# Performance work log

Hardware: AMD Instinct MI355X
Metric: run time of the kernel (lower is better)

Reference implementation:

```python
import jax, jax.numpy as jnp
import numpy as np

N, T, D, C = 32, 512, 1024, 120
EPS = 1e-12
SCALE = 2.0 * (D ** 0.5)


def setup_inputs() -> dict:
    key = jax.random.key(0)
    ks = jax.random.split(key, 16)
    inp = {
        'anc_perm_input': jax.random.normal(ks[0], (N, T, D), dtype=jnp.float32),
        'pos_perm_input': jax.random.normal(ks[1], (N, T, D), dtype=jnp.float32),
        'neg_perm_input': jax.random.normal(ks[2], (N, T, D), dtype=jnp.float32),
        'anc_src_key_padding_mask': jax.random.randint(ks[3], (N, T), 0, 2) == 1,
        'pos_src_key_padding_mask': jax.random.randint(ks[4], (N, T), 0, 2) == 1,
        'neg_src_key_padding_mask': jax.random.randint(ks[5], (N, T), 0, 2) == 1,
        # learned parameters (stored as (in, out); math-equivalent to torch x @ W.T)
        'W_attn': jax.random.normal(ks[6], (D, D), dtype=jnp.float32) * 0.02,
        'b_attn': jnp.zeros((D,), dtype=jnp.float32),
        'W1': jax.random.normal(ks[7], (D, D), dtype=jnp.float32) * 0.02,
        'b1': jnp.zeros((D,), dtype=jnp.float32),
        'W2': jax.random.normal(ks[8], (D, D), dtype=jnp.float32) * 0.02,
        'b2': jnp.zeros((D,), dtype=jnp.float32),
        'ln_g': jnp.ones((D,), dtype=jnp.float32),
        'ln_b': jnp.zeros((D,), dtype=jnp.float32),
        'W_last': jax.random.normal(ks[9], (D, C), dtype=jnp.float32) * 0.02,
        'b_last': jnp.zeros((C,), dtype=jnp.float32),
    }
    return inp


def _ntd_nd(x, mask, W_attn, b_attn, W1, b1, W2, b2, ln_g, ln_b, W_last, b_last):
    # x: (N,T,D); mask: (N,T) bool, True = padding
    w = x @ W_attn + b_attn                                   # (N,T,D)
    valid = ~mask                                             # (N,T)
    scores = jnp.einsum('btd,bsd->bts', w, w)                 # (N,T,T)
    scores = jnp.where(valid[:, :, None] & valid[:, None, :], scores, 0.0)
    s = jnp.sum(scores, axis=1) / SCALE                       # (N,T)
    s = jnp.where(mask, -jnp.inf, s)
    attn = jax.nn.softmax(s, axis=1)                          # (N,T)
    # proj_head: duplicate OrderedDict key => linear1 -> relu -> linear2 (no final act)
    proj = jax.nn.relu(x @ W1 + b1) @ W2 + b2                 # (N,T,D)
    pooled = jnp.einsum('bt,btd->bd', attn, proj)             # (N,D)
    mu = jnp.mean(pooled, axis=-1, keepdims=True)
    var = jnp.var(pooled, axis=-1, keepdims=True)
    normed = (pooled - mu) / jnp.sqrt(var + EPS) * ln_g + ln_b
    return jax.nn.relu(normed) @ W_last + b_last              # (N,C)


def reference(anc_perm_input, pos_perm_input, neg_perm_input,
              anc_src_key_padding_mask, pos_src_key_padding_mask, neg_src_key_padding_mask,
              W_attn, b_attn, W1, b1, W2, b2, ln_g, ln_b, W_last, b_last):
    params = (W_attn, b_attn, W1, b1, W2, b2, ln_g, ln_b, W_last, b_last)
    anc = _ntd_nd(anc_perm_input, anc_src_key_padding_mask, *params)
    pos = _ntd_nd(pos_perm_input, pos_src_key_padding_mask, *params)
    neg = _ntd_nd(neg_perm_input, neg_src_key_padding_mask, *params)
    return (anc, pos, neg)
```

## Files before the change

kernel.cpp:

```cpp
#include <hip/hip_runtime.h>
#include <hip/hip_bf16.h>
#include <math.h>

#define N_B 32
#define T_S 512
#define D_D 1024
#define C_C 120
#define ZB 96
#define SCALE 64.0f

typedef unsigned short u16;
typedef __attribute__((ext_vector_type(8))) short short8;
typedef __attribute__((ext_vector_type(8))) unsigned short ushort8;
typedef __attribute__((ext_vector_type(4))) float floatx4;

__device__ inline u16 f2bf(float f) {
    union { __hip_bfloat16 h; u16 u; } c; c.h = __float2bfloat16(f); return c.u;
}
__device__ inline float bf2f(u16 u) {
    union { unsigned i; float f; } c; c.i = ((unsigned)u) << 16; return c.f;
}

__device__ inline void gll16(const void* g, void* l) {
    __builtin_amdgcn_global_load_lds((const __attribute__((address_space(1))) void*)g,
                                     (__attribute__((address_space(3))) void*)l,
                                     16, 0, 0);
}

__device__ inline bool mask_is_i8(const int* mk) {
    bool i8 = false;
#pragma unroll
    for (int i = 0; i < 16; i++) {
        unsigned v = ((const unsigned*)mk)[i];
        if (v > 1u) i8 = true;
    }
    return i8;
}
__device__ inline int mask_val(const int* mk, int idx, bool i8) {
    return i8 ? (int)((const signed char*)mk)[idx] : mk[idx];
}

__global__ __launch_bounds__(512)
void k_scan(const int* m0, const int* m1, const int* m2,
            const float* __restrict__ W_attn, const float* __restrict__ W1,
            int* __restrict__ slotbase, int* __restrict__ cnts,
            int* __restrict__ gb, int* __restrict__ zblk,
            int* __restrict__ mtot, u16* __restrict__ xp,
            float* __restrict__ WT, u16* __restrict__ W1T,
            float4* __restrict__ zreg) {
    int zb = blockIdx.x;
    int tid = threadIdx.x;
    if (zb >= ZB) {
        int bx = zb - ZB;
        int tbx = bx & 31, tby = bx >> 5;
        __shared__ float tile[32][33];
        int tx = tid & 31, ty = tid >> 5;
#pragma unroll
        for (int j = 0; j < 32; j += 16)
            tile[ty + j][tx] = W_attn[(size_t)(tby*32 + ty + j)*D_D + tbx*32 + tx];
        __syncthreads();
#pragma unroll
        for (int j = 0; j < 32; j += 16)
            WT[(size_t)(tbx*32 + ty + j)*D_D + tby*32 + tx] = tile[tx][ty + j];
        __syncthreads();
#pragma unroll
        for (int j = 0; j < 32; j += 16)
            tile[ty + j][tx] = W1[(size_t)(tby*32 + ty + j)*D_D + tbx*32 + tx];
        __syncthreads();
#pragma unroll
        for (int j = 0; j < 32; j += 16)
            W1T[(size_t)(tbx*32 + ty + j)*D_D + tby*32 + tx] = f2bf(tile[tx][ty + j]);
        return;
    }
    {
        float4 zz4 = {0.f, 0.f, 0.f, 0.f};
        for (int i = zb * 512 + tid; i < (2 * 1024 * 1024 / 16); i += ZB * 512)
            zreg[i] = zz4;
    }
    bool i8_0 = mask_is_i8(m0), i8_1 = mask_is_i8(m1), i8_2 = mask_is_i8(m2);
    __shared__ unsigned short wc[ZB][8];
    __shared__ int scnt[ZB], sgb[ZB], stot;
    int wave = tid >> 6, lane = tid & 63;
#pragma unroll
    for (int it = 0; it < 12; it++) {
        int zb2 = wave * 12 + it;
        int z2 = zb2 >> 5, b2 = zb2 & 31;
        const int* mk = z2 == 0 ? m0 : (z2 == 1 ? m1 : m2);
        bool i8 = z2 == 0 ? i8_0 : (z2 == 1 ? i8_1 : i8_2);
        int c = 0;
        if (i8) {
            const signed char* p = (const signed char*)mk + b2 * T_S + lane * 8;
#pragma unroll
            for (int e = 0; e < 8; e++) c += (p[e] == 0);
        } else {
            const int* p = mk + b2 * T_S + lane * 8;
#pragma unroll
            for (int e = 0; e < 8; e++) c += (p[e] == 0);
        }
        c += __shfl_xor(c, 1, 64);
        c += __shfl_xor(c, 2, 64);
        c += __shfl_xor(c, 4, 64);
        if ((lane & 7) == 0) wc[zb2][lane >> 3] = (unsigned short)c;
    }
    __syncthreads();
    if (tid < ZB) {
        int s = 0;
#pragma unroll
        for (int c = 0; c < 8; c++) s += wc[tid][c];
        scnt[tid] = s;
    }
    __syncthreads();
    if (tid == 0) {
        int run = 0;
        for (int i = 0; i < ZB; i++) { sgb[i] = run; run += (scnt[i] + 63) & ~63; }
        stot = run;
    }
    __syncthreads();
    int cnt = scnt[zb], base = sgb[zb];
    if (tid == 0) {
        cnts[zb] = cnt; gb[zb] = base;
        int run = base;
#pragma unroll
        for (int c = 0; c < 8; c++) { slotbase[zb * 8 + c] = run; run += wc[zb][c]; }
        if (zb == ZB - 1) mtot[0] = stot;
    }
    int nb = (cnt + 63) >> 6;
    if (tid < nb) zblk[(base >> 6) + tid] = zb;
    int cend = (cnt + 63) & ~63;
    {
        u16* bp = xp + (size_t)(base + cnt) * D_D;
        int n8 = (cend - cnt) * (D_D / 8);
        ushort8 zz = {0,0,0,0,0,0,0,0};
        for (int i = tid; i < n8; i += 512)
            *(ushort8*)(bp + (size_t)i * 8) = zz;
    }
    if (zb == ZB - 1) {
        int tot = stot, tend = (tot + 255) & ~255;
        u16* bp = xp + (size_t)tot * D_D;
        int n8 = (tend - tot) * (D_D / 8);
        ushort8 zz = {0,0,0,0,0,0,0,0};
        for (int i = tid; i < n8; i += 512)
            *(ushort8*)(bp + (size_t)i * 8) = zz;
        if (tid < ((tend - tot) >> 6)) zblk[(tot >> 6) + tid] = 0;
    }
}

__global__ void k_prep(const float* x0, const float* x1, const float* x2,
                       const int* m0, const int* m1, const int* m2,
                       const int* __restrict__ slotbase,
                       float* __restrict__ xsum, u16* __restrict__ xp) {
    int idx = blockIdx.x;
    int tid = threadIdx.x;
    int chunk = idx & 7, zb = idx >> 3;
    int z = zb >> 5, b = zb & 31;
    const float* x = z == 0 ? x0 : (z == 1 ? x1 : x2);
    const int* mk = z == 0 ? m0 : (z == 1 ? m1 : m2);
    bool i8 = mask_is_i8(mk);
    int t0 = chunk * 64;
    __shared__ unsigned char s_list[64];
    __shared__ int s_cc;
    if (tid < 64) {
        bool v = (mask_val(mk, b * T_S + t0 + tid, i8) == 0);
        unsigned long long bal = __ballot(v);
        int pos = (int)__popcll(bal & ((1ull << tid) - 1ull));
        if (v) s_list[pos] = (unsigned char)tid;
        if (tid == 0) s_cc = (int)__popcll(bal);
    }
    __syncthreads();
    int cc = s_cc;
    int slot0 = slotbase[zb * 8 + chunk];
    const float4* xr = (const float4*)(x + (size_t)(b * T_S) * D_D);
    float4 acc = {0.f, 0.f, 0.f, 0.f};
#pragma unroll 4
    for (int j = 0; j < cc; j++) {
        int t = t0 + (int)s_list[j];
        float4 v = xr[(size_t)t * 256 + tid];
        union { __hip_bfloat162 h; ushort2 u; } c0, c1;
        c0.h = __float22bfloat162_rn({v.x, v.y});
        c1.h = __float22bfloat162_rn({v.z, v.w});
        ushort4 uu = {c0.u.x, c0.u.y, c1.u.x, c1.u.y};
        *(ushort4*)(xp + (size_t)(slot0 + j) * D_D + tid * 4) = uu;
        acc.x += v.x; acc.y += v.y; acc.z += v.z; acc.w += v.w;
    }
    float* xs = xsum + (size_t)zb * D_D + tid * 4;
    atomicAdd(xs + 0, acc.x); atomicAdd(xs + 1, acc.y);
    atomicAdd(xs + 2, acc.z); atomicAdd(xs + 3, acc.w);
}

__global__ void k_matvec(const float* __restrict__ W, const float* __restrict__ vin,
                         const float* __restrict__ bias, const int* __restrict__ bmul,
                         float scale, float* __restrict__ vout) {
    int z = blockIdx.z, bg = blockIdx.y;
    int och = blockIdx.x >> 3, kc = blockIdx.x & 7;
    int o = och * 256 + threadIdx.x;
    int brow = z * N_B + bg * 8;
    float acc[8] = {0.f, 0.f, 0.f, 0.f, 0.f, 0.f, 0.f, 0.f};
    if (kc == 0 && bias) {
        float bv = bias[o];
#pragma unroll
        for (int bb = 0; bb < 8; bb++)
            acc[bb] = bmul ? bv * (float)bmul[brow + bb] : bv;
    }
    const float* vi = vin + (size_t)brow * D_D + kc * 128;
    const float* Wp = W + (size_t)(kc * 128) * D_D + o;
#pragma unroll 4
    for (int i = 0; i < 128; i++) {
        float wv = Wp[(size_t)i * D_D];
#pragma unroll
        for (int bb = 0; bb < 8; bb++)
            acc[bb] += vi[(size_t)bb * D_D + i] * wv;
    }
#pragma unroll
    for (int bb = 0; bb < 8; bb++)
        atomicAdd(&vout[(size_t)(brow + bb) * D_D + o], acc[bb] * scale);
}

__global__ void k_dots(const u16* __restrict__ xp, const float* __restrict__ vs,
                       const int* __restrict__ zblk, const int* __restrict__ mtot,
                       float* __restrict__ sdot) {
    int t0 = blockIdx.x * 4;
    if (t0 >= mtot[0]) return;
    int t = t0 + (threadIdx.x >> 6);
    int lane = threadIdx.x & 63;
    int zb = zblk[t0 >> 6];
    const u16* xr = xp + (size_t)t * D_D;
    const float* vr = vs + (size_t)zb * D_D;
    float acc = 0.f;
#pragma unroll
    for (int i = 0; i < 2; i++) {
        short8 v = *(const short8*)(xr + i * 512 + lane * 8);
        const float* vp = vr + i * 512 + lane * 8;
        float4 a0 = *(const float4*)(vp);
        float4 a1 = *(const float4*)(vp + 4);
        acc += bf2f((u16)v[0]) * a0.x + bf2f((u16)v[1]) * a0.y
             + bf2f((u16)v[2]) * a0.z + bf2f((u16)v[3]) * a0.w
             + bf2f((u16)v[4]) * a1.x + bf2f((u16)v[5]) * a1.y
             + bf2f((u16)v[6]) * a1.z + bf2f((u16)v[7]) * a1.w;
    }
#pragma unroll
    for (int off = 32; off; off >>= 1) acc += __shfl_xor(acc, off, 64);
    if (lane == 0) sdot[t] = acc;
}

#define STAGE_TILE(buf, k0)                                                   \
    {                                                                         \
        _Pragma("unroll")                                                     \
        for (int i_ = 0; i_ < 4; i_++) {                                      \
            int r0_ = i_ * 64 + wave * 8;                                     \
            int rr_ = r0_ + srow;                                             \
            int gc_ = cp ^ srow;            \
            gll16(abase + (size_t)rr_ * D_D + (k0) + gc_ * 8,                 \
                  &As[buf][r0_ * 64]);                                        \
            gll16(bbase + (size_t)rr_ * D_D + (k0) + gc_ * 8,                 \
                  &Bs[buf][r0_ * 64]);                                        \
        }                                                                     \
    }

__global__ __launch_bounds__(512, 1)
void k_gemm_bf16(const u16* __restrict__ xp, const u16* __restrict__ W1T,
                 const float* __restrict__ b1, const float* __restrict__ sdot,
                 const int* __restrict__ cnts, const int* __restrict__ gb,
                 const int* __restrict__ zblk, const int* __restrict__ mtot,
                 float* __restrict__ rbuf) {
    int bid = blockIdx.x;
    int sub = bid & 31;
    int Mt = (bid >> 5) * 8 + (sub & 7);
    int Nt = sub >> 3;
    int row0 = Mt * 256, N0 = Nt * 256;
    if (row0 >= mtot[0]) return;

    __shared__ __align__(16) u16 As[2][256 * 64];
    __shared__ __align__(16) u16 Bs[2][256 * 64];
    __shared__ float sAttn[256];
    __shared__ float redm[8], reds[8];
    int tid = threadIdx.x;
    int wave = tid >> 6, lane = tid & 63;

    {
        int g0 = row0 >> 6;
        int prevzb = -1, czb_cnt = 0, czb_base = 0;
        float mx = 0.f, tot = 1.f;
#pragma unroll
        for (int g = 0; g < 4; g++) {
            int zbg = zblk[g0 + g];
            if (zbg != prevzb) {
                czb_cnt = cnts[zbg]; czb_base = gb[zbg];
                float v = (tid < czb_cnt) ? sdot[czb_base + tid] : -INFINITY;
                float m = v;
#pragma unroll
                for (int off = 32; off; off >>= 1) m = fmaxf(m, __shfl_xor(m, off, 64));
                if (lane == 0) redm[wave] = m;
                __syncthreads();
                m = redm[0];
#pragma unroll
                for (int k = 1; k < 8; k++) m = fmaxf(m, redm[k]);
                float e = __expf(v - m);
#pragma unroll
                for (int off = 32; off; off >>= 1) e += __shfl_xor(e, off, 64);
                if (lane == 0) reds[wave] = e;
                __syncthreads();
                float t_ = 0.f;
#pragma unroll
                for (int k = 0; k < 8; k++) t_ += reds[k];
                mx = m; tot = t_; prevzb = zbg;
            }
            if (tid < 64) {
                int row = row0 + g * 64 + tid;
                int tl = row - czb_base;
                float w = 0.f;
                if (tl < czb_cnt) w = __expf(sdot[row] - mx) / tot;
                sAttn[g * 64 + tid] = w;
            }
            __syncthreads();
        }
    }

    int wy = wave >> 2, wx = wave & 3;
    int q = lane >> 4, cidx = lane & 15;
    int srow = lane >> 3;
    int cp = lane & 7;

    floatx4 acc[8][4];
#pragma unroll
    for (int mi = 0; mi < 8; mi++)
#pragma unroll
        for (int ni = 0; ni < 4; ni++)
            acc[mi][ni] = (floatx4){0.f, 0.f, 0.f, 0.f};

    const u16* abase = xp + (size_t)row0 * D_D;
    const u16* bbase = W1T + (size_t)N0 * D_D;

    STAGE_TILE(0, 0)
    __syncthreads();
    int cur = 0;
#pragma unroll 2
    for (int kt = 0; kt < 16; kt++) {
        if (kt < 15) { STAGE_TILE(cur ^ 1, (kt + 1) << 6) }
        __builtin_amdgcn_sched_barrier(0);
#pragma unroll
        for (int ks = 0; ks < 2; ks++) {
            short8 a[8], bfr[4];
#pragma unroll
            for (int mi = 0; mi < 8; mi++) {
                int m = wy * 128 + mi * 16 + cidx;
                a[mi] = *(const short8*)&As[cur][m * 64 + ((((ks << 2) | q) ^ (m & 7)) << 3)];
            }
#pragma unroll
            for (int ni = 0; ni < 4; ni++) {
                int n = wx * 64 + ni * 16 + cidx;
                bfr[ni] = *(const short8*)&Bs[cur][n * 64 + ((((ks << 2) | q) ^ (n & 7)) << 3)];
            }
#pragma unroll
            for (int mi = 0; mi < 8; mi++)
#pragma unroll
                for (int ni = 0; ni < 4; ni++)
                    acc[mi][ni] = __builtin_amdgcn_mfma_f32_16x16x32_bf16(
                        a[mi], bfr[ni], acc[mi][ni], 0, 0, 0);
        }
        __syncthreads();
        cur ^= 1;
    }

    int zb0 = zblk[(row0 >> 6) + wy * 2];
    int zb1 = zblk[(row0 >> 6) + wy * 2 + 1];
#pragma unroll
    for (int ni = 0; ni < 4; ni++) {
        int ng = N0 + wx * 64 + ni * 16 + cidx;
        float b1v = b1[ng];
        float s0 = 0.f, s1 = 0.f;
#pragma unroll
        for (int mi = 0; mi < 8; mi++) {
            float part = 0.f;
#pragma unroll
            for (int rg = 0; rg < 4; rg++) {
                int ml = wy * 128 + mi * 16 + q * 4 + rg;
                float hv = fmaxf(acc[mi][ni][rg] + b1v, 0.f);
                part += hv * sAttn[ml];
            }
            if (mi < 4) s0 += part; else s1 += part;
        }
        s0 += __shfl_xor(s0, 16, 64); s0 += __shfl_xor(s0, 32, 64);
        s1 += __shfl_xor(s1, 16, 64); s1 += __shfl_xor(s1, 32, 64);
        if (lane < 16) {
            atomicAdd(&rbuf[(size_t)zb0 * D_D + ng], s0);
            atomicAdd(&rbuf[(size_t)zb1 * D_D + ng], s1);
        }
    }
}

__global__ void k_fin(const float* __restrict__ pooled, const float* __restrict__ ln_g,
                      const float* __restrict__ ln_b, const float* __restrict__ Wl,
                      const float* __restrict__ bl, float* __restrict__ out) {
    int zb = blockIdx.x;
    int tid = threadIdx.x;
    __shared__ float nr[D_D];
    __shared__ float redA[8], redB[8];
    __shared__ float ps[4][C_C];
    const float* p = pooled + (size_t)zb * D_D;
    int o0 = tid, o1 = tid + 512;
    float a0 = p[o0], a1 = p[o1];
    float s1 = a0 + a1, s2 = a0 * a0 + a1 * a1;
#pragma unroll
    for (int off = 32; off; off >>= 1) {
        s1 += __shfl_xor(s1, off, 64);
        s2 += __shfl_xor(s2, off, 64);
    }
    int w = tid >> 6;
    if ((tid & 63) == 0) { redA[w] = s1; redB[w] = s2; }
    __syncthreads();
    float t1 = 0.f, t2 = 0.f;
#pragma unroll
    for (int k = 0; k < 8; k++) { t1 += redA[k]; t2 += redB[k]; }
    float mu = t1 * (1.0f / D_D);
    float var = t2 * (1.0f / D_D) - mu * mu;
    float rstd = 1.0f / sqrtf(var + 1e-12f);
    nr[o0] = fmaxf((a0 - mu) * rstd * ln_g[o0] + ln_b[o0], 0.f);
    nr[o1] = fmaxf((a1 - mu) * rstd * ln_g[o1] + ln_b[o1], 0.f);
    __syncthreads();
    if (tid < 4 * C_C) {
        int seg = tid / C_C, c = tid - seg * C_C;
        const float* wp = Wl + (size_t)(seg * 256) * C_C + c;
        const float* np = nr + seg * 256;
        float acc = 0.f;
#pragma unroll 8
        for (int d = 0; d < 256; d++)
            acc += np[d] * wp[(size_t)d * C_C];
        ps[seg][c] = acc;
    }
    __syncthreads();
    if (tid < C_C)
        out[(size_t)zb * C_C + tid] =
            bl[tid] + ps[0][tid] + ps[1][tid] + ps[2][tid] + ps[3][tid];
}

extern "C" void kernel_launch(void* const* d_in, const int* in_sizes, int n_in,
                              void* d_out, int out_size, void* d_ws, size_t ws_size,
                              hipStream_t stream) {
    const float* x0 = (const float*)d_in[0];
    const float* x1 = (const float*)d_in[1];
    const float* x2 = (const float*)d_in[2];
    const int* m0 = (const int*)d_in[3];
    const int* m1 = (const int*)d_in[4];
    const int* m2 = (const int*)d_in[5];
    const float* W_attn = (const float*)d_in[6];
    const float* b_attn = (const float*)d_in[7];
    const float* W1 = (const float*)d_in[8];
    const float* b1 = (const float*)d_in[9];
    const float* W2 = (const float*)d_in[10];
    const float* b2 = (const float*)d_in[11];
    const float* ln_g = (const float*)d_in[12];
    const float* ln_b = (const float*)d_in[13];
    const float* W_last = (const float*)d_in[14];
    const float* b_last = (const float*)d_in[15];
    float* out = (float*)d_out;

    char* wsb = (char*)d_ws;
    const size_t MB = 1 << 20;
    float* WT     = (float*)(wsb);
    u16*   W1T    = (u16*)  (wsb + 4 * MB);
    float* xsum   = (float*)(wsb + 6 * MB);
    float* rbuf   = (float*)(wsb + 6 * MB + 393216);
    float* wsum   = (float*)(wsb + 6 * MB + 786432);
    float* vs     = (float*)(wsb + 6 * MB + 1179648);
    float* pooled = (float*)(wsb + 6 * MB + 1572864);
    float* sdot   = (float*)(wsb + 8 * MB);
    int*   slotb  = (int*)  (wsb + 8 * MB + 524288);
    int*   cnts   = (int*)  (wsb + 8 * MB + 528384);
    int*   gb     = (int*)  (wsb + 8 * MB + 532480);
    int*   mtot   = (int*)  (wsb + 8 * MB + 536576);
    int*   zblk   = (int*)  (wsb + 8 * MB + 540672);
    u16*   xp     = (u16*)  (wsb + 9 * MB);

    k_scan  <<<ZB + 1024, 512, 0, stream>>>(m0, m1, m2, W_attn, W1,
                                            slotb, cnts, gb, zblk, mtot,
                                            xp, WT, W1T, (float4*)(wsb + 6 * MB));
    k_prep  <<<768, 256, 0, stream>>>(x0, x1, x2, m0, m1, m2, slotb, xsum, xp);
    k_matvec<<<dim3(32, 4, 3), 256, 0, stream>>>(W_attn, xsum, b_attn, cnts, 1.0f, wsum);
    k_matvec<<<dim3(32, 4, 3), 256, 0, stream>>>(WT, wsum, nullptr, nullptr, 1.0f / SCALE, vs);
    k_dots  <<<12288, 256, 0, stream>>>(xp, vs, zblk, mtot, sdot);
    k_gemm_bf16<<<768, 512, 0, stream>>>(xp, W1T, b1, sdot, cnts, gb, zblk, mtot, rbuf);
    k_matvec<<<dim3(32, 4, 3), 256, 0, stream>>>(W2, rbuf, b2, nullptr, 1.0f, pooled);
    k_fin   <<<ZB, 512, 0, stream>>>(pooled, ln_g, ln_b, W_last, b_last, out);
}
```

Measured before the change: 375.6 us.

## Merge matvec/dots and W2/LN-final stages into cooperative kernels with grid sync

Replaces the two attention matvec launches and the dots launch with one cooperative kernel that separates the stages with grid.sync. Likewise, the W2 matvec and the LayerNorm/final linear are merged into a second cooperative kernel, where the matvec now uses 512-thread blocks. The goal is to remove kernel launch gaps and the tail effects of small grids. In exchange it pays for grid-wide barriers, and the dots stage runs on a fixed 768-block persistent loop instead of 12288 blocks.

```diff
diff --git a/kernel.cpp b/kernel.cpp
--- a/kernel.cpp
+++ b/kernel.cpp
@@ -1,6 +1,9 @@
 #include <hip/hip_runtime.h>
 #include <hip/hip_bf16.h>
+#include <hip/hip_cooperative_groups.h>
 #include <math.h>
+
+namespace cg = cooperative_groups;
 
 #define N_B 32
 #define T_S 512
@@ -187,59 +190,85 @@
     atomicAdd(xs + 2, acc.z); atomicAdd(xs + 3, acc.w);
 }
 
-__global__ void k_matvec(const float* __restrict__ W, const float* __restrict__ vin,
-                         const float* __restrict__ bias, const int* __restrict__ bmul,
-                         float scale, float* __restrict__ vout) {
-    int z = blockIdx.z, bg = blockIdx.y;
-    int och = blockIdx.x >> 3, kc = blockIdx.x & 7;
-    int o = och * 256 + threadIdx.x;
-    int brow = z * N_B + bg * 8;
-    float acc[8] = {0.f, 0.f, 0.f, 0.f, 0.f, 0.f, 0.f, 0.f};
-    if (kc == 0 && bias) {
-        float bv = bias[o];
+__global__ __launch_bounds__(256)
+void k_mid(const float* __restrict__ W, const float* __restrict__ WT,
+           const float* __restrict__ b_attn, const int* __restrict__ cnts,
+           const float* __restrict__ xsum, float* __restrict__ wsum,
+           float* __restrict__ vs, const u16* __restrict__ xp,
+           const int* __restrict__ zblk, const int* __restrict__ mtot,
+           float* __restrict__ sdot) {
+    cg::grid_group grid = cg::this_grid();
+    int bid = blockIdx.x, tid = threadIdx.x;
+    if (bid < 384) {
+        int x = bid & 31, bg = (bid >> 5) & 3, z = bid >> 7;
+        int och = x >> 3, kc = x & 7;
+        int o = och * 256 + tid;
+        int brow = z * N_B + bg * 8;
+        float acc[8] = {0.f, 0.f, 0.f, 0.f, 0.f, 0.f, 0.f, 0.f};
+        if (kc == 0) {
+            float bv = b_attn[o];
+#pragma unroll
+            for (int bb = 0; bb < 8; bb++)
+                acc[bb] = bv * (float)cnts[brow + bb];
+        }
+        const float* vi = xsum + (size_t)brow * D_D + kc * 128;
+        const float* Wp = W + (size_t)(kc * 128) * D_D + o;
+#pragma unroll 4
+        for (int i = 0; i < 128; i++) {
+            float wv = Wp[(size_t)i * D_D];
+#pragma unroll
+            for (int bb = 0; bb < 8; bb++)
+                acc[bb] += vi[(size_t)bb * D_D + i] * wv;
+        }
 #pragma unroll
         for (int bb = 0; bb < 8; bb++)
-            acc[bb] = bmul ? bv * (float)bmul[brow + bb] : bv;
-    }
-    const float* vi = vin + (size_t)brow * D_D + kc * 128;
-    const float* Wp = W + (size_t)(kc * 128) * D_D + o;
+            atomicAdd(&wsum[(size_t)(brow + bb) * D_D + o], acc[bb]);
+    }
+    grid.sync();
+    if (bid < 384) {
+        int x = bid & 31, bg = (bid >> 5) & 3, z = bid >> 7;
+        int och = x >> 3, kc = x & 7;
+        int o = och * 256 + tid;
+        int brow = z * N_B + bg * 8;
+        float acc[8] = {0.f, 0.f, 0.f, 0.f, 0.f, 0.f, 0.f, 0.f};
+        const float* vi = wsum + (size_t)brow * D_D + kc * 128;
+        const float* Wp = WT + (size_t)(kc * 128) * D_D + o;
 #pragma unroll 4
-    for (int i = 0; i < 128; i++) {
-        float wv = Wp[(size_t)i * D_D];
+        for (int i = 0; i < 128; i++) {
+            float wv = Wp[(size_t)i * D_D];
+#pragma unroll
+            for (int bb = 0; bb < 8; bb++)
+                acc[bb] += vi[(size_t)bb * D_D + i] * wv;
+        }
 #pragma unroll
         for (int bb = 0; bb < 8; bb++)
-            acc[bb] += vi[(size_t)bb * D_D + i] * wv;
-    }
-#pragma unroll
-    for (int bb = 0; bb < 8; bb++)
-        atomicAdd(&vout[(size_t)(brow + bb) * D_D + o], acc[bb] * scale);
-}
-
-__global__ void k_dots(const u16* __restrict__ xp, const float* __restrict__ vs,
-                       const int* __restrict__ zblk, const int* __restrict__ mtot,
-                       float* __restrict__ sdot) {
-    int t0 = blockIdx.x * 4;
-    if (t0 >= mtot[0]) return;
-    int t = t0 + (threadIdx.x >> 6);
-    int lane = threadIdx.x & 63;
-    int zb = zblk[t0 >> 6];
-    const u16* xr = xp + (size_t)t * D_D;
-    const float* vr = vs + (size_t)zb * D_D;
-    float acc = 0.f;
-#pragma unroll
-    for (int i = 0; i < 2; i++) {
-        short8 v = *(const short8*)(xr + i * 512 + lane * 8);
-        const float* vp = vr + i * 512 + lane * 8;
-        float4 a0 = *(const float4*)(vp);
-        float4 a1 = *(const float4*)(vp + 4);
-        acc += bf2f((u16)v[0]) * a0.x + bf2f((u16)v[1]) * a0.y
-             + bf2f((u16)v[2]) * a0.z + bf2f((u16)v[3]) * a0.w
-             + bf2f((u16)v[4]) * a1.x + bf2f((u16)v[5]) * a1.y
-             + bf2f((u16)v[6]) * a1.z + bf2f((u16)v[7]) * a1.w;
-    }
-#pragma unroll
-    for (int off = 32; off; off >>= 1) acc += __shfl_xor(acc, off, 64);
-    if (lane == 0) sdot[t] = acc;
+            atomicAdd(&vs[(size_t)(brow + bb) * D_D + o], acc[bb] * (1.0f / SCALE));
+    }
+    grid.sync();
+    int lane = tid & 63;
+    int mt = mtot[0];
+#pragma unroll 2
+    for (int t0 = bid * 4; t0 < mt; t0 += 768 * 4) {
+        int t = t0 + (tid >> 6);
+        int zb = zblk[t0 >> 6];
+        const u16* xr = xp + (size_t)t * D_D;
+        const float* vr = vs + (size_t)zb * D_D;
+        float acc = 0.f;
+#pragma unroll
+        for (int i = 0; i < 2; i++) {
+            short8 v = *(const short8*)(xr + i * 512 + lane * 8);
+            const float* vp = vr + i * 512 + lane * 8;
+            float4 a0 = *(const float4*)(vp);
+            float4 a1 = *(const float4*)(vp + 4);
+            acc += bf2f((u16)v[0]) * a0.x + bf2f((u16)v[1]) * a0.y
+                 + bf2f((u16)v[2]) * a0.z + bf2f((u16)v[3]) * a0.w
+                 + bf2f((u16)v[4]) * a1.x + bf2f((u16)v[5]) * a1.y
+                 + bf2f((u16)v[6]) * a1.z + bf2f((u16)v[7]) * a1.w;
+        }
+#pragma unroll
+        for (int off = 32; off; off >>= 1) acc += __shfl_xor(acc, off, 64);
+        if (lane == 0) sdot[t] = acc;
+    }
 }
 
 #define STAGE_TILE(buf, k0)                                                   \
@@ -388,49 +417,80 @@
     }
 }
 
-__global__ void k_fin(const float* __restrict__ pooled, const float* __restrict__ ln_g,
-                      const float* __restrict__ ln_b, const float* __restrict__ Wl,
-                      const float* __restrict__ bl, float* __restrict__ out) {
-    int zb = blockIdx.x;
-    int tid = threadIdx.x;
+__global__ __launch_bounds__(512)
+void k_tail2(const float* __restrict__ rbuf, const float* __restrict__ W2,
+             const float* __restrict__ b2, float* __restrict__ pooled,
+             const float* __restrict__ ln_g, const float* __restrict__ ln_b,
+             const float* __restrict__ Wl, const float* __restrict__ bl,
+             float* __restrict__ out) {
+    cg::grid_group grid = cg::this_grid();
+    int bid = blockIdx.x, tid = threadIdx.x;
     __shared__ float nr[D_D];
     __shared__ float redA[8], redB[8];
     __shared__ float ps[4][C_C];
-    const float* p = pooled + (size_t)zb * D_D;
-    int o0 = tid, o1 = tid + 512;
-    float a0 = p[o0], a1 = p[o1];
-    float s1 = a0 + a1, s2 = a0 * a0 + a1 * a1;
-#pragma unroll
-    for (int off = 32; off; off >>= 1) {
-        s1 += __shfl_xor(s1, off, 64);
-        s2 += __shfl_xor(s2, off, 64);
-    }
-    int w = tid >> 6;
-    if ((tid & 63) == 0) { redA[w] = s1; redB[w] = s2; }
-    __syncthreads();
-    float t1 = 0.f, t2 = 0.f;
-#pragma unroll
-    for (int k = 0; k < 8; k++) { t1 += redA[k]; t2 += redB[k]; }
-    float mu = t1 * (1.0f / D_D);
-    float var = t2 * (1.0f / D_D) - mu * mu;
-    float rstd = 1.0f / sqrtf(var + 1e-12f);
-    nr[o0] = fmaxf((a0 - mu) * rstd * ln_g[o0] + ln_b[o0], 0.f);
-    nr[o1] = fmaxf((a1 - mu) * rstd * ln_g[o1] + ln_b[o1], 0.f);
-    __syncthreads();
-    if (tid < 4 * C_C) {
-        int seg = tid / C_C, c = tid - seg * C_C;
-        const float* wp = Wl + (size_t)(seg * 256) * C_C + c;
-        const float* np = nr + seg * 256;
-        float acc = 0.f;
+    {
+        int x = bid & 15, bg = (bid >> 4) & 3, z = bid >> 6;
+        int och = x >> 3, kc = x & 7;
+        int o = och * 512 + tid;
+        int brow = z * N_B + bg * 8;
+        float acc[8] = {0.f, 0.f, 0.f, 0.f, 0.f, 0.f, 0.f, 0.f};
+        if (kc == 0) {
+            float bv = b2[o];
+#pragma unroll
+            for (int bb = 0; bb < 8; bb++) acc[bb] = bv;
+        }
+        const float* vi = rbuf + (size_t)brow * D_D + kc * 128;
+        const float* Wp = W2 + (size_t)(kc * 128) * D_D + o;
+#pragma unroll 4
+        for (int i = 0; i < 128; i++) {
+            float wv = Wp[(size_t)i * D_D];
+#pragma unroll
+            for (int bb = 0; bb < 8; bb++)
+                acc[bb] += vi[(size_t)bb * D_D + i] * wv;
+        }
+#pragma unroll
+        for (int bb = 0; bb < 8; bb++)
+            atomicAdd(&pooled[(size_t)(brow + bb) * D_D + o], acc[bb]);
+    }
+    grid.sync();
+    if (bid < 96) {
+        int zb = bid;
+        const float* p = pooled + (size_t)zb * D_D;
+        int o0 = tid, o1 = tid + 512;
+        float a0 = p[o0], a1 = p[o1];
+        float s1 = a0 + a1, s2 = a0 * a0 + a1 * a1;
+#pragma unroll
+        for (int off = 32; off; off >>= 1) {
+            s1 += __shfl_xor(s1, off, 64);
+            s2 += __shfl_xor(s2, off, 64);
+        }
+        int w = tid >> 6;
+        if ((tid & 63) == 0) { redA[w] = s1; redB[w] = s2; }
+        __syncthreads();
+        float t1 = 0.f, t2 = 0.f;
+#pragma unroll
+        for (int k = 0; k < 8; k++) { t1 += redA[k]; t2 += redB[k]; }
+        float mu = t1 * (1.0f / D_D);
+        float var = t2 * (1.0f / D_D) - mu * mu;
+        float rstd = 1.0f / sqrtf(var + 1e-12f);
+        nr[o0] = fmaxf((a0 - mu) * rstd * ln_g[o0] + ln_b[o0], 0.f);
+        nr[o1] = fmaxf((a1 - mu) * rstd * ln_g[o1] + ln_b[o1], 0.f);
+        __syncthreads();
+        if (tid < 4 * C_C) {
+            int seg = tid / C_C, c = tid - seg * C_C;
+            const float* wp = Wl + (size_t)(seg * 256) * C_C + c;
+            const float* np = nr + seg * 256;
+            float acc = 0.f;
 #pragma unroll 8
-        for (int d = 0; d < 256; d++)
-            acc += np[d] * wp[(size_t)d * C_C];
-        ps[seg][c] = acc;
-    }
-    __syncthreads();
-    if (tid < C_C)
-        out[(size_t)zb * C_C + tid] =
-            bl[tid] + ps[0][tid] + ps[1][tid] + ps[2][tid] + ps[3][tid];
+            for (int d = 0; d < 256; d++)
+                acc += np[d] * wp[(size_t)d * C_C];
+            ps[seg][c] = acc;
+        }
+        __syncthreads();
+        if (tid < C_C)
+            out[(size_t)zb * C_C + tid] =
+                bl[tid] + ps[0][tid] + ps[1][tid] + ps[2][tid] + ps[3][tid];
+    }
 }
 
 extern "C" void kernel_launch(void* const* d_in, const int* in_sizes, int n_in,
@@ -475,10 +535,17 @@
                                             slotb, cnts, gb, zblk, mtot,
                                             xp, WT, W1T, (float4*)(wsb + 6 * MB));
     k_prep  <<<768, 256, 0, stream>>>(x0, x1, x2, m0, m1, m2, slotb, xsum, xp);
-    k_matvec<<<dim3(32, 4, 3), 256, 0, stream>>>(W_attn, xsum, b_attn, cnts, 1.0f, wsum);
-    k_matvec<<<dim3(32, 4, 3), 256, 0, stream>>>(WT, wsum, nullptr, nullptr, 1.0f / SCALE, vs);
-    k_dots  <<<12288, 256, 0, stream>>>(xp, vs, zblk, mtot, sdot);
+    {
+        void* a[] = {(void*)&W_attn, (void*)&WT, (void*)&b_attn, (void*)&cnts,
+                     (void*)&xsum, (void*)&wsum, (void*)&vs, (void*)&xp,
+                     (void*)&zblk, (void*)&mtot, (void*)&sdot};
+        hipLaunchCooperativeKernel((void*)k_mid, dim3(768), dim3(256), a, 0, stream);
+    }
     k_gemm_bf16<<<768, 512, 0, stream>>>(xp, W1T, b1, sdot, cnts, gb, zblk, mtot, rbuf);
-    k_matvec<<<dim3(32, 4, 3), 256, 0, stream>>>(W2, rbuf, b2, nullptr, 1.0f, pooled);
-    k_fin   <<<ZB, 512, 0, stream>>>(pooled, ln_g, ln_b, W_last, b_last, out);
-}
+    {
+        void* a[] = {(void*)&rbuf, (void*)&W2, (void*)&b2, (void*)&pooled,
+                     (void*)&ln_g, (void*)&ln_b, (void*)&W_last, (void*)&b_last,
+                     (void*)&out};
+        hipLaunchCooperativeKernel((void*)k_tail2, dim3(192), dim3(512), a, 0, stream);
+    }
+}
```

Measured after the change: 585.8 us. 55.9% more time.
